# Performance work log

Hardware: AMD Instinct MI355X
Metric: run time of the kernel (lower is better)

Reference implementation:

```python
import jax, jax.numpy as jnp
import numpy as np

D_MODEL = 1024
NUM_SLOTS = 4096
MIN_K = 8
MAX_K = 32


def setup_inputs() -> dict:
    key = jax.random.key(0)
    k1, k2, k3 = jax.random.split(key, 3)
    x = jax.random.normal(k1, (4, 1024, D_MODEL), dtype=jnp.float32)
    param_pool = 0.02 * jax.random.normal(k2, (NUM_SLOTS, D_MODEL), dtype=jnp.float32)
    w_router = 0.02 * jax.random.normal(k3, (D_MODEL, NUM_SLOTS), dtype=jnp.float32)
    return {"x": x, "param_pool": param_pool, "w_router": w_router}


def _route(x, w_router):
    # Router: linear projection to slot logits, softmax, dynamic top-k in [MIN_K, MAX_K].
    logits = jnp.einsum('bsd,dn->bsn', x, w_router)           # [B,S,N]
    probs = jax.nn.softmax(logits, axis=-1)
    top_probs, indices = jax.lax.top_k(probs, MAX_K)          # [B,S,K]
    # dynamic k: always keep first MIN_K slots; keep up to MAX_K while prob > uniform
    pos = jnp.arange(MAX_K)
    keep = (pos < MIN_K) | (top_probs > (1.0 / NUM_SLOTS))    # [B,S,K] bool
    keep_f = keep.astype(top_probs.dtype)
    masked = top_probs * keep_f
    weights = masked / (jnp.sum(masked, axis=-1, keepdims=True) + 1e-9)
    # load-balancing aux loss: N * sum(mean_prob_per_slot * frac_tokens_routed_per_slot)
    mean_probs = jnp.mean(probs, axis=(0, 1))                 # [N]
    counts = jnp.zeros((NUM_SLOTS,), dtype=jnp.float32).at[indices.reshape(-1)].add(keep_f.reshape(-1))
    frac = counts / (jnp.sum(keep_f) + 1e-9)
    aux_loss = NUM_SLOTS * jnp.sum(mean_probs * frac)
    return indices, weights, keep, aux_loss


def reference(x, param_pool, w_router):
    indices, weights, keep, aux_loss = _route(x, w_router)
    selected_params = param_pool[indices]                      # [B,S,K,D] gather
    proj = jnp.einsum('bsd,bskd->bsk', x, selected_params)     # per-token dot scores
    weighted_proj = proj * weights
    output = jnp.einsum('bsk,bskd->bsd', weighted_proj, selected_params)
    flat_indices = indices.reshape(-1)
    flat_keep = keep.reshape(-1)
    touched = jnp.zeros((NUM_SLOTS,), dtype=jnp.bool_).at[flat_indices].max(flat_keep)
    active_count = jnp.sum(touched)
    return (output, aux_loss, active_count)
```

## Files before the change

kernel.cpp:

```cpp
#include <hip/hip_runtime.h>
#include <math.h>
#include <stdint.h>

#define D_MODEL   1024
#define NUM_SLOTS 4096
#define N_TOKENS  4096
#define MIN_K     8
#define MAX_K     32
#define KP        1024
#define NSTEP     32

typedef _Float16 f16x8 __attribute__((ext_vector_type(8)));
typedef _Float16 f16x4 __attribute__((ext_vector_type(4)));
typedef _Float16 h2    __attribute__((ext_vector_type(2)));
typedef float    f32x4 __attribute__((ext_vector_type(4)));

__device__ __forceinline__ void gload16(const void* g, void* l) {
    __builtin_amdgcn_global_load_lds((const __attribute__((address_space(1))) void*)g,
                                     (__attribute__((address_space(3))) void*)l,
                                     16, 0, 0);
}

__device__ __forceinline__ h2 as_h2(uint32_t u) {
    union { uint32_t u; h2 h; } c; c.u = u; return c.h;
}
__device__ __forceinline__ uint32_t h2pack(float a, float b) {
    union { uint32_t u; h2 h; } c; c.h.x = (_Float16)a; c.h.y = (_Float16)b; return c.u;
}

__device__ __forceinline__ uint32_t ford(float f) {
    uint32_t b = __float_as_uint(f);
    return b ^ (uint32_t)(((int32_t)b >> 31) | 0x80000000);
}

__global__ __launch_bounds__(256) void pack_all(const float* __restrict__ x,
                                                const float* __restrict__ w,
                                                const float* __restrict__ pool,
                                                _Float16* __restrict__ A,
                                                _Float16* __restrict__ BT,
                                                uint32_t* __restrict__ poolh,
                                                float* __restrict__ clr,
                                                int* __restrict__ failcnt) {
    __shared__ float tile[64][65];
    const int bid = blockIdx.x;
    const int tid = threadIdx.x;

    if (bid < 4096) {
        if (bid < 32) clr[bid * 256 + tid] = 0.f;
        if (bid == 32 && tid == 0) { failcnt[0] = 0; failcnt[1] = 0; }
        const int i = bid * 256 + tid;
        const float4 v = reinterpret_cast<const float4*>(x)[i];
        const int t = i >> 8;
        const int d = (i & 255) << 2;
        f16x4 hi;
        hi[0] = (_Float16)v.x; hi[1] = (_Float16)v.y;
        hi[2] = (_Float16)v.z; hi[3] = (_Float16)v.w;
        *(f16x4*)(A + (size_t)t * KP + d) = hi;
    } else if (bid < 5120) {
        const int b2 = bid - 4096;
        const int n0 = (b2 & 63) * 64;
        const int k0 = (b2 >> 6) * 64;
        {
            const int c  = tid & 63;
            const int r0 = tid >> 6;
#pragma unroll
            for (int i = 0; i < 16; ++i) {
                const int r = r0 * 16 + i;
                tile[r][c] = w[(size_t)(k0 + r) * NUM_SLOTS + n0 + c];
            }
        }
        __syncthreads();
        const int nl  = tid >> 2;
        const int kl0 = (tid & 3) * 16;
        _Float16* rowp = BT + (size_t)(n0 + nl) * KP + k0;
#pragma unroll
        for (int j4 = 0; j4 < 16; j4 += 4) {
            f16x4 hi;
#pragma unroll
            for (int u = 0; u < 4; ++u)
                hi[u] = (_Float16)tile[kl0 + j4 + u][nl];
            *(f16x4*)(rowp + kl0 + j4) = hi;
        }
    } else {
        const size_t i = (size_t)(bid - 5120) * 256 + tid;
        const float4* s4 = reinterpret_cast<const float4*>(pool);
        const float4 a = s4[2 * i];
        const float4 b = s4[2 * i + 1];
        uint4 u;
        u.x = h2pack(a.x, a.y);
        u.y = h2pack(a.z, a.w);
        u.z = h2pack(b.x, b.y);
        u.w = h2pack(b.z, b.w);
        reinterpret_cast<uint4*>(poolh)[i] = u;
    }
}

#define STAGE_A(NXT, S2) \
    gload16(gA0 + (size_t)(S2) * 32, (void*)(AsF + (NXT) * 8192 + tid * 8)); \
    gload16(gA1 + (size_t)(S2) * 32, (void*)(AsF + (NXT) * 8192 + 4096 + tid * 8));
#define STAGE_B(NXT, S2) \
    gload16(gB0 + (size_t)(S2) * 32, (void*)(BsF + (NXT) * 8192 + tid * 8)); \
    gload16(gB1 + (size_t)(S2) * 32, (void*)(BsF + (NXT) * 8192 + 4096 + tid * 8));

#define MM(AF, M) \
    acc[M][0] = __builtin_amdgcn_mfma_f32_16x16x32_f16(AF, bf0, acc[M][0], 0, 0, 0); \
    acc[M][1] = __builtin_amdgcn_mfma_f32_16x16x32_f16(AF, bf1, acc[M][1], 0, 0, 0); \
    acc[M][2] = __builtin_amdgcn_mfma_f32_16x16x32_f16(AF, bf2, acc[M][2], 0, 0, 0); \
    acc[M][3] = __builtin_amdgcn_mfma_f32_16x16x32_f16(AF, bf3, acc[M][3], 0, 0, 0);

#define GSTEP(S, CUR, NXT) do { \
    const _Float16* a_ = AsF + (CUR) * 8192; \
    const _Float16* b_ = BsF + (CUR) * 8192; \
    f16x8 bf0 = *(const f16x8*)(b_ + offB0); \
    f16x8 bf1 = *(const f16x8*)(b_ + offB1); \
    f16x8 bf2 = *(const f16x8*)(b_ + offB2); \
    f16x8 bf3 = *(const f16x8*)(b_ + offB3); \
    f16x8 a0 = *(const f16x8*)(a_ + offA0); \
    f16x8 a1 = *(const f16x8*)(a_ + offA1); \
    f16x8 a2 = *(const f16x8*)(a_ + offA2); \
    f16x8 a3 = *(const f16x8*)(a_ + offA3); \
    if ((S) + 2 < NSTEP) { STAGE_A(NXT, (S) + 2) } \
    asm volatile("" ::: "memory"); \
    __builtin_amdgcn_s_barrier(); \
    __builtin_amdgcn_s_setprio(1); \
    MM(a0, 0) MM(a1, 1) MM(a2, 2) MM(a3, 3) \
    __builtin_amdgcn_s_setprio(0); \
    asm volatile("" ::: "memory"); \
    __builtin_amdgcn_s_barrier(); \
    a0 = *(const f16x8*)(a_ + offA4); \
    a1 = *(const f16x8*)(a_ + offA5); \
    a2 = *(const f16x8*)(a_ + offA6); \
    a3 = *(const f16x8*)(a_ + offA7); \
    if ((S) + 2 < NSTEP) { STAGE_B(NXT, (S) + 2) } \
    asm volatile("" ::: "memory"); \
    __builtin_amdgcn_s_barrier(); \
    __builtin_amdgcn_s_setprio(1); \
    MM(a0, 4) MM(a1, 5) MM(a2, 6) MM(a3, 7) \
    __builtin_amdgcn_s_setprio(0); \
    if ((S) < NSTEP - 2) { asm volatile("s_waitcnt vmcnt(4)" ::: "memory"); } \
    else                 { asm volatile("s_waitcnt vmcnt(0)" ::: "memory"); } \
    __builtin_amdgcn_s_barrier(); \
} while (0)

__global__ __launch_bounds__(512, 2) void gemm256(const _Float16* __restrict__ A,
                                                  const _Float16* __restrict__ BT,
                                                  float* __restrict__ C,
                                                  int nbm) {
    __shared__ _Float16 AsF[4 * 8192];
    __shared__ _Float16 BsF[4 * 8192];
    const int tid  = threadIdx.x;
    const int lane = tid & 63;
    const int wv   = tid >> 6;
    const int wm   = wv >> 2;
    const int wn   = wv & 3;

    int brow, bcol;
    {
        const int bid = blockIdx.x;
        if (nbm == 16) {
            const int xcd = bid & 7;
            const int l   = bid >> 3;
            brow = (xcd & 3) * 4 + (l & 3);
            bcol = (xcd >> 2) * 8 + (l >> 2);
        } else {
            brow = bid >> 4;
            bcol = bid & 15;
        }
    }
    const size_t bm = (size_t)brow * 256;
    const size_t bn = (size_t)bcol * 256;

    const int rowA = tid >> 2;
    const int slot = tid & 3;
    const int sswz = slot ^ ((rowA >> 1) & 3);
    const _Float16* gA0 = A  + (bm + rowA) * (size_t)KP + sswz * 8;
    const _Float16* gA1 = A  + (bm + rowA + 128) * (size_t)KP + sswz * 8;
    const _Float16* gB0 = BT + (bn + rowA) * (size_t)KP + sswz * 8;
    const _Float16* gB1 = BT + (bn + rowA + 128) * (size_t)KP + sswz * 8;

    int offA0, offA1, offA2, offA3, offA4, offA5, offA6, offA7;
    int offB0, offB1, offB2, offB3;
    {
        const int r15 = lane & 15, ls = lane >> 4;
#define AOFF(M) (((wm) * 128 + (M) * 16 + r15) * 32 + \
                 ((ls ^ ((((wm) * 128 + (M) * 16 + r15) >> 1) & 3)) * 8))
#define BOFF(N) (((wn) * 64 + (N) * 16 + r15) * 32 + \
                 ((ls ^ ((((wn) * 64 + (N) * 16 + r15) >> 1) & 3)) * 8))
        offA0 = AOFF(0); offA1 = AOFF(1); offA2 = AOFF(2); offA3 = AOFF(3);
        offA4 = AOFF(4); offA5 = AOFF(5); offA6 = AOFF(6); offA7 = AOFF(7);
        offB0 = BOFF(0); offB1 = BOFF(1); offB2 = BOFF(2); offB3 = BOFF(3);
#undef AOFF
#undef BOFF
    }

    f32x4 acc[8][4] = {};

    STAGE_A(0, 0) STAGE_B(0, 0)
    STAGE_A(1, 1) STAGE_B(1, 1)
    asm volatile("s_waitcnt vmcnt(4)" ::: "memory");
    __builtin_amdgcn_s_barrier();

    for (int s4 = 0; s4 < NSTEP; s4 += 4) {
        GSTEP(s4 + 0, 0, 2);
        GSTEP(s4 + 1, 1, 3);
        GSTEP(s4 + 2, 2, 0);
        GSTEP(s4 + 3, 3, 1);
    }

    const size_t crow = bm + wm * 128 + ((lane >> 4) << 2);
    const size_t ccol = bn + wn * 64 + (lane & 15);
#pragma unroll
    for (int m = 0; m < 8; ++m)
#pragma unroll
        for (int r = 0; r < 4; ++r) {
            float* cp = C + (crow + m * 16 + r) * (size_t)NUM_SLOTS + ccol;
#pragma unroll
            for (int n = 0; n < 4; ++n) cp[n * 16] = acc[m][n][r];
        }
}

#define RECOMP(G, A, B, Cc, D) do { \
    uint32_t t0 = (msk & (1u << (A)))  ? k##A  : 0u; \
    uint32_t t1 = (msk & (1u << (B)))  ? k##B  : 0u; \
    uint32_t t2 = (msk & (1u << (Cc))) ? k##Cc : 0u; \
    uint32_t t3 = (msk & (1u << (D)))  ? k##D  : 0u; \
    t0 = t0 > t1 ? t0 : t1; t2 = t2 > t3 ? t2 : t3; \
    gm##G = t0 > t2 ? t0 : t2; } while (0)

#define XROUND(IT) do { \
    uint32_t best = gm0; \
    if (gm1 > best) best = gm1; \
    if (gm2 > best) best = gm2; \
    if (gm3 > best) best = gm3; \
    uint32_t wb = best; \
    _Pragma("unroll") \
    for (int o = 32; o; o >>= 1) { \
        const uint32_t p = __shfl_xor(wb, o); \
        if (p > wb) wb = p; \
    } \
    if (lane == (IT)) kept = wb; \
    if (best == wb) { \
        const int idx = 4095 - (int)(wb & 0xFFFu); \
        const int rem = idx - kb; \
        const int jj = rem >> 8; \
        msk &= ~(1u << (4 * jj + (rem & 3))); \
        switch (jj) { \
            case 0:  RECOMP(0, 0, 1, 2, 3); break; \
            case 1:  RECOMP(1, 4, 5, 6, 7); break; \
            case 2:  RECOMP(2, 8, 9, 10, 11); break; \
            default: RECOMP(3, 12, 13, 14, 15); break; \
        } \
    } \
} while (0)

#define MAKEKEYS(E0, E1, E2, E3) \
    k0  = (ford((E0).x) & 0xFFFFF000u) | (uint32_t)(4095 - (kb + 0)); \
    k1  = (ford((E0).y) & 0xFFFFF000u) | (uint32_t)(4095 - (kb + 1)); \
    k2  = (ford((E0).z) & 0xFFFFF000u) | (uint32_t)(4095 - (kb + 2)); \
    k3  = (ford((E0).w) & 0xFFFFF000u) | (uint32_t)(4095 - (kb + 3)); \
    k4  = (ford((E1).x) & 0xFFFFF000u) | (uint32_t)(4095 - (kb + 256)); \
    k5  = (ford((E1).y) & 0xFFFFF000u) | (uint32_t)(4095 - (kb + 257)); \
    k6  = (ford((E1).z) & 0xFFFFF000u) | (uint32_t)(4095 - (kb + 258)); \
    k7  = (ford((E1).w) & 0xFFFFF000u) | (uint32_t)(4095 - (kb + 259)); \
    k8  = (ford((E2).x) & 0xFFFFF000u) | (uint32_t)(4095 - (kb + 512)); \
    k9  = (ford((E2).y) & 0xFFFFF000u) | (uint32_t)(4095 - (kb + 513)); \
    k10 = (ford((E2).z) & 0xFFFFF000u) | (uint32_t)(4095 - (kb + 514)); \
    k11 = (ford((E2).w) & 0xFFFFF000u) | (uint32_t)(4095 - (kb + 515)); \
    k12 = (ford((E3).x) & 0xFFFFF000u) | (uint32_t)(4095 - (kb + 768)); \
    k13 = (ford((E3).y) & 0xFFFFF000u) | (uint32_t)(4095 - (kb + 769)); \
    k14 = (ford((E3).z) & 0xFFFFF000u) | (uint32_t)(4095 - (kb + 770)); \
    k15 = (ford((E3).w) & 0xFFFFF000u) | (uint32_t)(4095 - (kb + 771));

#define PROJ_AND_OUT(TOK) do { \
    const uint4* xA = reinterpret_cast<const uint4*>(Af + (size_t)(TOK) * D_MODEL); \
    const uint4 xq0 = xA[lane]; \
    const uint4 xq1 = xA[lane + 64]; \
    const h2 xh0 = as_h2(xq0.x), xh1 = as_h2(xq0.y); \
    const h2 xh2 = as_h2(xq0.z), xh3 = as_h2(xq0.w); \
    const h2 xh4 = as_h2(xq1.x), xh5 = as_h2(xq1.y); \
    const h2 xh6 = as_h2(xq1.z), xh7 = as_h2(xq1.w); \
    float4 oa0 = {0,0,0,0}, ob0 = {0,0,0,0}, oa1 = {0,0,0,0}, ob1 = {0,0,0,0}; \
    _Pragma("unroll") \
    for (int ii = 0; ii < 8; ++ii) { \
        const int   i     = w * 8 + ii; \
        const int   slotg = __shfl(slotv, i); \
        const float wgt   = __shfl(wgtl, i); \
        if (wgt != 0.f) { \
            const uint4* pr = reinterpret_cast<const uint4*>(poolh + (size_t)slotg * (D_MODEL / 2)); \
            const uint4 q0 = pr[lane]; \
            const uint4 q1 = pr[lane + 64]; \
            const h2 p0 = as_h2(q0.x), p1 = as_h2(q0.y); \
            const h2 p2 = as_h2(q0.z), p3 = as_h2(q0.w); \
            const h2 p4 = as_h2(q1.x), p5 = as_h2(q1.y); \
            const h2 p6 = as_h2(q1.z), p7 = as_h2(q1.w); \
            h2 acc2 = xh0 * p0; \
            acc2 = xh1 * p1 + acc2; \
            acc2 = xh2 * p2 + acc2; \
            acc2 = xh3 * p3 + acc2; \
            acc2 = xh4 * p4 + acc2; \
            acc2 = xh5 * p5 + acc2; \
            acc2 = xh6 * p6 + acc2; \
            acc2 = xh7 * p7 + acc2; \
            float d = (float)acc2.x + (float)acc2.y; \
            _Pragma("unroll") \
            for (int o = 32; o; o >>= 1) d += __shfl_xor(d, o); \
            const float wp = d * wgt; \
            oa0.x = fmaf(wp, (float)p0.x, oa0.x); oa0.y = fmaf(wp, (float)p0.y, oa0.y); \
            oa0.z = fmaf(wp, (float)p1.x, oa0.z); oa0.w = fmaf(wp, (float)p1.y, oa0.w); \
            ob0.x = fmaf(wp, (float)p2.x, ob0.x); ob0.y = fmaf(wp, (float)p2.y, ob0.y); \
            ob0.z = fmaf(wp, (float)p3.x, ob0.z); ob0.w = fmaf(wp, (float)p3.y, ob0.w); \
            oa1.x = fmaf(wp, (float)p4.x, oa1.x); oa1.y = fmaf(wp, (float)p4.y, oa1.y); \
            oa1.z = fmaf(wp, (float)p5.x, oa1.z); oa1.w = fmaf(wp, (float)p5.y, oa1.w); \
            ob1.x = fmaf(wp, (float)p6.x, ob1.x); ob1.y = fmaf(wp, (float)p6.y, ob1.y); \
            ob1.z = fmaf(wp, (float)p7.x, ob1.z); ob1.w = fmaf(wp, (float)p7.y, ob1.w); \
        } \
    } \
    { \
        float4* op = reinterpret_cast<float4*>(s_union + w * 1024); \
        op[2 * lane]       = oa0; \
        op[2 * lane + 1]   = ob0; \
        op[2 * lane + 128] = oa1; \
        op[2 * lane + 129] = ob1; \
    } \
    __syncthreads(); \
    float4 r = {0, 0, 0, 0}; \
    _Pragma("unroll") \
    for (int ww = 0; ww < 4; ++ww) { \
        const float4 vv = reinterpret_cast<const float4*>(s_union + ww * 1024)[tid]; \
        r.x += vv.x; r.y += vv.y; r.z += vv.z; r.w += vv.w; \
    } \
    reinterpret_cast<float4*>(out + (size_t)(TOK) * D_MODEL)[tid] = r; \
} while (0)

__global__ __launch_bounds__(256) void router_kernel(
    const float* __restrict__ logits,
    const _Float16* __restrict__ Af,
    const uint32_t* __restrict__ poolh,
    float* __restrict__ out,
    float2* __restrict__ minv,
    float* __restrict__ counts,
    int* __restrict__ failcnt,
    int* __restrict__ faillist) {
    __shared__ float    s_union[NUM_SLOTS];
    __shared__ uint32_t s_cand[68];
    __shared__ float    s_redv[4];

    const int tid  = threadIdx.x;
    const int w    = tid >> 6;
    const int lane = tid & 63;
    const int wseg = w << 10;
    const int t    = blockIdx.x;

    const float4* lrow4 =
        reinterpret_cast<const float4*>(logits + (size_t)t * NUM_SLOTS + wseg);

    float4 lv0, lv1, lv2, lv3;
    lv0 = lrow4[lane];
    lv1 = lrow4[lane + 64];
    lv2 = lrow4[lane + 128];
    lv3 = lrow4[lane + 192];
    reinterpret_cast<float4*>(s_union + wseg)[lane]       = lv0;
    reinterpret_cast<float4*>(s_union + wseg)[lane + 64]  = lv1;
    reinterpret_cast<float4*>(s_union + wseg)[lane + 128] = lv2;
    reinterpret_cast<float4*>(s_union + wseg)[lane + 192] = lv3;
    float lmax = fmaxf(fmaxf(fmaxf(lv0.x, lv0.y), fmaxf(lv0.z, lv0.w)),
                       fmaxf(fmaxf(lv1.x, lv1.y), fmaxf(lv1.z, lv1.w)));
    lmax = fmaxf(lmax, fmaxf(fmaxf(lv2.x, lv2.y), fmaxf(lv2.z, lv2.w)));
    lmax = fmaxf(lmax, fmaxf(fmaxf(lv3.x, lv3.y), fmaxf(lv3.z, lv3.w)));
#pragma unroll
    for (int o = 32; o; o >>= 1) lmax = fmaxf(lmax, __shfl_xor(lmax, o));
    if (lane == 0) s_redv[w] = lmax;
    __syncthreads();
    const float m = fmaxf(fmaxf(s_redv[0], s_redv[1]), fmaxf(s_redv[2], s_redv[3]));
    __syncthreads();

    float lsum;
    {
        float4 ev0, ev1, ev2, ev3;
        ev0.x = __expf(lv0.x - m); ev0.y = __expf(lv0.y - m);
        ev0.z = __expf(lv0.z - m); ev0.w = __expf(lv0.w - m);
        ev1.x = __expf(lv1.x - m); ev1.y = __expf(lv1.y - m);
        ev1.z = __expf(lv1.z - m); ev1.w = __expf(lv1.w - m);
        ev2.x = __expf(lv2.x - m); ev2.y = __expf(lv2.y - m);
        ev2.z = __expf(lv2.z - m); ev2.w = __expf(lv2.w - m);
        ev3.x = __expf(lv3.x - m); ev3.y = __expf(lv3.y - m);
        ev3.z = __expf(lv3.z - m); ev3.w = __expf(lv3.w - m);
        lsum = (ev0.x + ev0.y + ev0.z + ev0.w) + (ev1.x + ev1.y + ev1.z + ev1.w) +
               (ev2.x + ev2.y + ev2.z + ev2.w) + (ev3.x + ev3.y + ev3.z + ev3.w);
    }
#pragma unroll
    for (int o = 32; o; o >>= 1) lsum += __shfl_xor(lsum, o);
    if (lane == 0) s_redv[w] = lsum;
    __syncthreads();
    const float inv = 1.0f / (s_redv[0] + s_redv[1] + s_redv[2] + s_redv[3]);
    if (tid == 0) minv[t] = make_float2(m, inv);

    const int kb = wseg + 4 * lane;
    uint32_t k0, k1, k2, k3, k4, k5, k6, k7;
    uint32_t k8, k9, k10, k11, k12, k13, k14, k15;
    MAKEKEYS(lv0, lv1, lv2, lv3)

    uint32_t msk = 0xFFFFu;
    uint32_t gm0, gm1, gm2, gm3;
    RECOMP(0, 0, 1, 2, 3); RECOMP(1, 4, 5, 6, 7);
    RECOMP(2, 8, 9, 10, 11); RECOMP(3, 12, 13, 14, 15);

    uint32_t kept = 0;
    for (int it = 0; it < 16; ++it) { XROUND(it); }

    {
        uint32_t best = gm0;
        if (gm1 > best) best = gm1;
        if (gm2 > best) best = gm2;
        if (gm3 > best) best = gm3;
#pragma unroll
        for (int o = 32; o; o >>= 1) {
            const uint32_t p = __shfl_xor(best, o);
            if (p > best) best = p;
        }
        if (lane == 0) s_cand[64 + w] = best;
    }
    if (lane < 16) s_cand[w * 16 + lane] = kept;
    __syncthreads();

    uint32_t v0 = s_cand[lane];
#pragma unroll
    for (int k = 2; k <= 64; k <<= 1) {
#pragma unroll
        for (int j = k >> 1; j > 0; j >>= 1) {
            const bool jl = (lane & j) == 0;
            const uint32_t p = __shfl_xor(v0, j);
            const bool km = ((lane & k) == 0) == jl;
            v0 = ((p > v0) == km) ? p : v0;
        }
    }

    const uint32_t th = __shfl(v0, 31);
    uint32_t mw = s_cand[64];
    {
        const uint32_t m1 = s_cand[65], m2 = s_cand[66], m3 = s_cand[67];
        if (m1 > mw) mw = m1;
        if (m2 > mw) mw = m2;
        if (m3 > mw) mw = m3;
    }
    if (th < mw) {
        if (tid == 0) {
            const int fi = atomicAdd(failcnt, 1);
            faillist[fi] = t;
        }
        return;
    }

    const int slotv = 4095 - (int)(v0 & 0xFFFu);
    float pv = 0.f;
    if (lane < 32) pv = __expf(s_union[slotv] - m) * inv;
    const bool kp = (lane < MIN_K) || (pv > (1.0f / 4096.0f));
    float wsum = kp ? pv : 0.f;
#pragma unroll
    for (int o = 32; o; o >>= 1) wsum += __shfl_xor(wsum, o);
    const float wgtl = kp ? pv / (wsum + 1e-9f) : 0.f;
    if (w == 0 && lane < 32 && kp) atomicAdd(&counts[slotv], 1.0f);
    __syncthreads();

    PROJ_AND_OUT(t);
}

__global__ __launch_bounds__(256) void router_fixup(
    const float* __restrict__ logits,
    const _Float16* __restrict__ Af,
    const uint32_t* __restrict__ poolh,
    float* __restrict__ out,
    const float2* __restrict__ minv,
    float* __restrict__ counts,
    const int* __restrict__ failcnt,
    const int* __restrict__ faillist) {
    __shared__ float    s_union[NUM_SLOTS];
    __shared__ uint32_t s_cand[128];

    const int tid  = threadIdx.x;
    const int w    = tid >> 6;
    const int lane = tid & 63;
    const int wseg = w << 10;
    const int n    = failcnt[0];

    for (int fi = blockIdx.x; fi < n; fi += gridDim.x) {
        const int t = faillist[fi];
        const float4* lrow4 =
            reinterpret_cast<const float4*>(logits + (size_t)t * NUM_SLOTS + wseg);
        const float4 lv0 = lrow4[lane];
        const float4 lv1 = lrow4[lane + 64];
        const float4 lv2 = lrow4[lane + 128];
        const float4 lv3 = lrow4[lane + 192];
        reinterpret_cast<float4*>(s_union + wseg)[lane]       = lv0;
        reinterpret_cast<float4*>(s_union + wseg)[lane + 64]  = lv1;
        reinterpret_cast<float4*>(s_union + wseg)[lane + 128] = lv2;
        reinterpret_cast<float4*>(s_union + wseg)[lane + 192] = lv3;
        const float2 mv = minv[t];
        const float m = mv.x, inv = mv.y;

        const int kb = wseg + 4 * lane;
        uint32_t k0, k1, k2, k3, k4, k5, k6, k7;
        uint32_t k8, k9, k10, k11, k12, k13, k14, k15;
        MAKEKEYS(lv0, lv1, lv2, lv3)

        uint32_t msk = 0xFFFFu;
        uint32_t gm0, gm1, gm2, gm3;
        RECOMP(0, 0, 1, 2, 3); RECOMP(1, 4, 5, 6, 7);
        RECOMP(2, 8, 9, 10, 11); RECOMP(3, 12, 13, 14, 15);

        uint32_t kept = 0;
        for (int it = 0; it < 32; ++it) { XROUND(it); }
        if (lane < 32) s_cand[w * 32 + lane] = kept;
        __syncthreads();

        uint32_t v0 = s_cand[lane];
        uint32_t v1 = s_cand[64 + lane];
#pragma unroll
        for (int k = 2; k <= 128; k <<= 1) {
#pragma unroll
            for (int j = k >> 1; j > 0; j >>= 1) {
                if (j == 64) {
                    const uint32_t a = v0 > v1 ? v0 : v1;
                    const uint32_t b = v0 > v1 ? v1 : v0;
                    v0 = a; v1 = b;
                } else {
                    const bool jl = (lane & j) == 0;
                    {
                        const uint32_t p = __shfl_xor(v0, j);
                        const bool km = ((lane & k) == 0) == jl;
                        v0 = ((p > v0) == km) ? p : v0;
                    }
                    {
                        const uint32_t p = __shfl_xor(v1, j);
                        const bool km = (((lane + 64) & k) == 0) == jl;
                        v1 = ((p > v1) == km) ? p : v1;
                    }
                }
            }
        }

        const int slotv = 4095 - (int)(v0 & 0xFFFu);
        float pv = 0.f;
        if (lane < 32) pv = __expf(s_union[slotv] - m) * inv;
        const bool kp = (lane < MIN_K) || (pv > (1.0f / 4096.0f));
        float wsum = kp ? pv : 0.f;
#pragma unroll
        for (int o = 32; o; o >>= 1) wsum += __shfl_xor(wsum, o);
        const float wgtl = kp ? pv / (wsum + 1e-9f) : 0.f;
        if (w == 0 && lane < 32 && kp) atomicAdd(&counts[slotv], 1.0f);
        __syncthreads();

        PROJ_AND_OUT(t);
        __syncthreads();
    }
}

__global__ __launch_bounds__(256) void colsum_lg(const float* __restrict__ logits,
                                                 const float2* __restrict__ minv,
                                                 float* __restrict__ colsum) {
    const int tid = threadIdx.x;
    const int s0  = blockIdx.x * 1024;
    const int t0  = blockIdx.y * 64;
    float a0 = 0.f, a1 = 0.f, a2 = 0.f, a3 = 0.f;
    for (int t = 0; t < 64; ++t) {
        const float2 mv = minv[t0 + t];
        const float4 v = reinterpret_cast<const float4*>(
            logits + (size_t)(t0 + t) * NUM_SLOTS + s0)[tid];
        a0 = fmaf(__expf(v.x - mv.x), mv.y, a0);
        a1 = fmaf(__expf(v.y - mv.x), mv.y, a1);
        a2 = fmaf(__expf(v.z - mv.x), mv.y, a2);
        a3 = fmaf(__expf(v.w - mv.x), mv.y, a3);
    }
    const int c = s0 + 4 * tid;
    atomicAdd(&colsum[c + 0], a0);
    atomicAdd(&colsum[c + 1], a1);
    atomicAdd(&colsum[c + 2], a2);
    atomicAdd(&colsum[c + 3], a3);
}

__global__ __launch_bounds__(256) void finalize_kernel(
    const float* __restrict__ counts,
    const float* __restrict__ colsum,
    float* __restrict__ out2) {
    __shared__ float s_tot[4], s_act[4], s_dot[4];
    const int tid = threadIdx.x;
    float tot = 0.f, act = 0.f, dot = 0.f;
#pragma unroll
    for (int j = 0; j < 16; ++j) {
        const int i = j * 256 + tid;
        const float c = counts[i];
        tot += c;
        act += (c > 0.f) ? 1.f : 0.f;
        dot += colsum[i] * c;
    }
#pragma unroll
    for (int o = 32; o; o >>= 1) {
        tot += __shfl_xor(tot, o);
        act += __shfl_xor(act, o);
        dot += __shfl_xor(dot, o);
    }
    if ((tid & 63) == 0) {
        s_tot[tid >> 6] = tot; s_act[tid >> 6] = act; s_dot[tid >> 6] = dot;
    }
    __syncthreads();
    if (tid == 0) {
        const float T  = s_tot[0] + s_tot[1] + s_tot[2] + s_tot[3];
        const float A  = s_act[0] + s_act[1] + s_act[2] + s_act[3];
        const float Dt = s_dot[0] + s_dot[1] + s_dot[2] + s_dot[3];
        out2[0] = Dt / (T + 1e-9f);
        out2[1] = A;
    }
}

extern "C" void kernel_launch(void* const* d_in, const int* in_sizes, int n_in,
                              void* d_out, int out_size, void* d_ws, size_t ws_size,
                              hipStream_t stream) {
    const float* x    = (const float*)d_in[0];
    const float* pool = (const float*)d_in[1];
    const float* w    = (const float*)d_in[2];
    float* out = (float*)d_out;

    const size_t MB = 1024 * 1024;
    char* ws = (char*)d_ws;
    float*     colsum   = (float*)ws;
    float*     counts   = (float*)(ws + 16 * 1024);
    float2*    minv     = (float2*)(ws + 32 * 1024);
    int*       failcnt  = (int*)(ws + 64 * 1024);
    int*       faillist = (int*)(ws + 68 * 1024);
    uint32_t*  poolh    = (uint32_t*)(ws + 128 * 1024);
    _Float16*  Apack    = (_Float16*)(ws + 128 * 1024 + 8 * MB);
    _Float16*  Bpack    = (_Float16*)(ws + 128 * 1024 + 16 * MB);
    float*     logits   = (float*)(ws + 128 * 1024 + 24 * MB);

    pack_all<<<7168, 256, 0, stream>>>(x, w, pool, Apack, Bpack, poolh,
                                       colsum, failcnt);

    gemm256<<<16 * 16, 512, 0, stream>>>(Apack, Bpack, logits, 16);

    router_kernel<<<N_TOKENS, 256, 0, stream>>>(logits, Apack, poolh, out,
                                                minv, counts, failcnt, faillist);

    router_fixup<<<64, 256, 0, stream>>>(logits, Apack, poolh, out,
                                         minv, counts, failcnt, faillist);

    colsum_lg<<<dim3(NUM_SLOTS / 1024, N_TOKENS / 64), 256, 0, stream>>>(
        logits, minv, colsum);

    finalize_kernel<<<1, 256, 0, stream>>>(counts, colsum, out + (out_size - 2));
}
```

Measured before the change: 149.7 us.

## Store router logits as fp16 and merge fixup with finalize kernel

The GEMM now writes the 4096x4096 logits matrix in fp16 instead of fp32, which halves the write traffic and the later reads by the router and colsum kernels. The fixup kernel is merged with the finalize step using a last-block atomic counter, removing one launch. colsum now runs before fixup. Storing logits in fp16 costs precision, which can change top-k selection among near-tied probabilities and alter the softmax values.

Measured after the change: 146.2 us. 2.4% less time.

```diff
diff --git a/kernel.cpp b/kernel.cpp
--- a/kernel.cpp
+++ b/kernel.cpp
@@ -144,7 +144,7 @@
 
 __global__ __launch_bounds__(512, 2) void gemm256(const _Float16* __restrict__ A,
                                                   const _Float16* __restrict__ BT,
-                                                  float* __restrict__ C,
+                                                  _Float16* __restrict__ C,
                                                   int nbm) {
     __shared__ _Float16 AsF[4 * 8192];
     __shared__ _Float16 BsF[4 * 8192];
@@ -213,9 +213,9 @@
     for (int m = 0; m < 8; ++m)
 #pragma unroll
         for (int r = 0; r < 4; ++r) {
-            float* cp = C + (crow + m * 16 + r) * (size_t)NUM_SLOTS + ccol;
-#pragma unroll
-            for (int n = 0; n < 4; ++n) cp[n * 16] = acc[m][n][r];
+            _Float16* cp = C + (crow + m * 16 + r) * (size_t)NUM_SLOTS + ccol;
+#pragma unroll
+            for (int n = 0; n < 4; ++n) cp[n * 16] = (_Float16)acc[m][n][r];
         }
 }
 
@@ -252,6 +252,25 @@
         } \
     } \
 } while (0)
+
+#define LOADLV(TOK) \
+    const uint2* lrow2 = reinterpret_cast<const uint2*>(logits + (size_t)(TOK) * NUM_SLOTS + wseg); \
+    float4 lv0, lv1, lv2, lv3; \
+    { \
+        const uint2 u0 = lrow2[lane]; \
+        const uint2 u1 = lrow2[lane + 64]; \
+        const uint2 u2 = lrow2[lane + 128]; \
+        const uint2 u3 = lrow2[lane + 192]; \
+        h2 ha, hb; \
+        ha = as_h2(u0.x); hb = as_h2(u0.y); \
+        lv0 = make_float4((float)ha.x, (float)ha.y, (float)hb.x, (float)hb.y); \
+        ha = as_h2(u1.x); hb = as_h2(u1.y); \
+        lv1 = make_float4((float)ha.x, (float)ha.y, (float)hb.x, (float)hb.y); \
+        ha = as_h2(u2.x); hb = as_h2(u2.y); \
+        lv2 = make_float4((float)ha.x, (float)ha.y, (float)hb.x, (float)hb.y); \
+        ha = as_h2(u3.x); hb = as_h2(u3.y); \
+        lv3 = make_float4((float)ha.x, (float)ha.y, (float)hb.x, (float)hb.y); \
+    }
 
 #define MAKEKEYS(E0, E1, E2, E3) \
     k0  = (ford((E0).x) & 0xFFFFF000u) | (uint32_t)(4095 - (kb + 0)); \
@@ -333,7 +352,7 @@
 } while (0)
 
 __global__ __launch_bounds__(256) void router_kernel(
-    const float* __restrict__ logits,
+    const _Float16* __restrict__ logits,
     const _Float16* __restrict__ Af,
     const uint32_t* __restrict__ poolh,
     float* __restrict__ out,
@@ -351,14 +370,8 @@
     const int wseg = w << 10;
     const int t    = blockIdx.x;
 
-    const float4* lrow4 =
-        reinterpret_cast<const float4*>(logits + (size_t)t * NUM_SLOTS + wseg);
-
-    float4 lv0, lv1, lv2, lv3;
-    lv0 = lrow4[lane];
-    lv1 = lrow4[lane + 64];
-    lv2 = lrow4[lane + 128];
-    lv3 = lrow4[lane + 192];
+    LOADLV(t)
+
     reinterpret_cast<float4*>(s_union + wseg)[lane]       = lv0;
     reinterpret_cast<float4*>(s_union + wseg)[lane + 64]  = lv1;
     reinterpret_cast<float4*>(s_union + wseg)[lane + 128] = lv2;
@@ -465,17 +478,45 @@
     PROJ_AND_OUT(t);
 }
 
-__global__ __launch_bounds__(256) void router_fixup(
-    const float* __restrict__ logits,
+__global__ __launch_bounds__(256) void colsum_lg(const _Float16* __restrict__ logits,
+                                                 const float2* __restrict__ minv,
+                                                 float* __restrict__ colsum) {
+    const int tid = threadIdx.x;
+    const int s0  = blockIdx.x * 1024;
+    const int t0  = blockIdx.y * 64;
+    float a0 = 0.f, a1 = 0.f, a2 = 0.f, a3 = 0.f;
+    for (int t = 0; t < 64; ++t) {
+        const float2 mv = minv[t0 + t];
+        const uint2 v = reinterpret_cast<const uint2*>(
+            logits + (size_t)(t0 + t) * NUM_SLOTS + s0)[tid];
+        const h2 va = as_h2(v.x), vb = as_h2(v.y);
+        a0 = fmaf(__expf((float)va.x - mv.x), mv.y, a0);
+        a1 = fmaf(__expf((float)va.y - mv.x), mv.y, a1);
+        a2 = fmaf(__expf((float)vb.x - mv.x), mv.y, a2);
+        a3 = fmaf(__expf((float)vb.y - mv.x), mv.y, a3);
+    }
+    const int c = s0 + 4 * tid;
+    atomicAdd(&colsum[c + 0], a0);
+    atomicAdd(&colsum[c + 1], a1);
+    atomicAdd(&colsum[c + 2], a2);
+    atomicAdd(&colsum[c + 3], a3);
+}
+
+__global__ __launch_bounds__(256) void fixup_fin(
+    const _Float16* __restrict__ logits,
     const _Float16* __restrict__ Af,
     const uint32_t* __restrict__ poolh,
     float* __restrict__ out,
     const float2* __restrict__ minv,
     float* __restrict__ counts,
-    const int* __restrict__ failcnt,
-    const int* __restrict__ faillist) {
+    float* __restrict__ colsum,
+    int* __restrict__ failcnt,
+    const int* __restrict__ faillist,
+    float* __restrict__ out2) {
     __shared__ float    s_union[NUM_SLOTS];
     __shared__ uint32_t s_cand[128];
+    __shared__ float    s_tot[4], s_act[4], s_dot[4];
+    __shared__ int      s_last;
 
     const int tid  = threadIdx.x;
     const int w    = tid >> 6;
@@ -485,12 +526,7 @@
 
     for (int fi = blockIdx.x; fi < n; fi += gridDim.x) {
         const int t = faillist[fi];
-        const float4* lrow4 =
-            reinterpret_cast<const float4*>(logits + (size_t)t * NUM_SLOTS + wseg);
-        const float4 lv0 = lrow4[lane];
-        const float4 lv1 = lrow4[lane + 64];
-        const float4 lv2 = lrow4[lane + 128];
-        const float4 lv3 = lrow4[lane + 192];
+        LOADLV(t)
         reinterpret_cast<float4*>(s_union + wseg)[lane]       = lv0;
         reinterpret_cast<float4*>(s_union + wseg)[lane + 64]  = lv1;
         reinterpret_cast<float4*>(s_union + wseg)[lane + 128] = lv2;
@@ -553,62 +589,40 @@
         PROJ_AND_OUT(t);
         __syncthreads();
     }
-}
-
-__global__ __launch_bounds__(256) void colsum_lg(const float* __restrict__ logits,
-                                                 const float2* __restrict__ minv,
-                                                 float* __restrict__ colsum) {
-    const int tid = threadIdx.x;
-    const int s0  = blockIdx.x * 1024;
-    const int t0  = blockIdx.y * 64;
-    float a0 = 0.f, a1 = 0.f, a2 = 0.f, a3 = 0.f;
-    for (int t = 0; t < 64; ++t) {
-        const float2 mv = minv[t0 + t];
-        const float4 v = reinterpret_cast<const float4*>(
-            logits + (size_t)(t0 + t) * NUM_SLOTS + s0)[tid];
-        a0 = fmaf(__expf(v.x - mv.x), mv.y, a0);
-        a1 = fmaf(__expf(v.y - mv.x), mv.y, a1);
-        a2 = fmaf(__expf(v.z - mv.x), mv.y, a2);
-        a3 = fmaf(__expf(v.w - mv.x), mv.y, a3);
-    }
-    const int c = s0 + 4 * tid;
-    atomicAdd(&colsum[c + 0], a0);
-    atomicAdd(&colsum[c + 1], a1);
-    atomicAdd(&colsum[c + 2], a2);
-    atomicAdd(&colsum[c + 3], a3);
-}
-
-__global__ __launch_bounds__(256) void finalize_kernel(
-    const float* __restrict__ counts,
-    const float* __restrict__ colsum,
-    float* __restrict__ out2) {
-    __shared__ float s_tot[4], s_act[4], s_dot[4];
-    const int tid = threadIdx.x;
-    float tot = 0.f, act = 0.f, dot = 0.f;
-#pragma unroll
-    for (int j = 0; j < 16; ++j) {
-        const int i = j * 256 + tid;
-        const float c = counts[i];
-        tot += c;
-        act += (c > 0.f) ? 1.f : 0.f;
-        dot += colsum[i] * c;
-    }
-#pragma unroll
-    for (int o = 32; o; o >>= 1) {
-        tot += __shfl_xor(tot, o);
-        act += __shfl_xor(act, o);
-        dot += __shfl_xor(dot, o);
-    }
-    if ((tid & 63) == 0) {
-        s_tot[tid >> 6] = tot; s_act[tid >> 6] = act; s_dot[tid >> 6] = dot;
-    }
+
+    __threadfence();
     __syncthreads();
-    if (tid == 0) {
-        const float T  = s_tot[0] + s_tot[1] + s_tot[2] + s_tot[3];
-        const float A  = s_act[0] + s_act[1] + s_act[2] + s_act[3];
-        const float Dt = s_dot[0] + s_dot[1] + s_dot[2] + s_dot[3];
-        out2[0] = Dt / (T + 1e-9f);
-        out2[1] = A;
+    if (tid == 0) s_last = (atomicAdd(&failcnt[1], 1) == (int)gridDim.x - 1) ? 1 : 0;
+    __syncthreads();
+    if (s_last) {
+        __threadfence();
+        float tot = 0.f, act = 0.f, dot = 0.f;
+#pragma unroll
+        for (int j = 0; j < 16; ++j) {
+            const int i = j * 256 + tid;
+            const float c  = atomicAdd(&counts[i], 0.f);
+            const float cs = colsum[i];
+            tot += c;
+            act += (c > 0.f) ? 1.f : 0.f;
+            dot += cs * c;
+        }
+#pragma unroll
+        for (int o = 32; o; o >>= 1) {
+            tot += __shfl_xor(tot, o);
+            act += __shfl_xor(act, o);
+            dot += __shfl_xor(dot, o);
+        }
+        if ((tid & 63) == 0) {
+            s_tot[tid >> 6] = tot; s_act[tid >> 6] = act; s_dot[tid >> 6] = dot;
+        }
+        __syncthreads();
+        if (tid == 0) {
+            const float T  = s_tot[0] + s_tot[1] + s_tot[2] + s_tot[3];
+            const float A  = s_act[0] + s_act[1] + s_act[2] + s_act[3];
+            const float Dt = s_dot[0] + s_dot[1] + s_dot[2] + s_dot[3];
+            out2[0] = Dt / (T + 1e-9f);
+            out2[1] = A;
+        }
     }
 }
 
@@ -630,7 +644,7 @@
     uint32_t*  poolh    = (uint32_t*)(ws + 128 * 1024);
     _Float16*  Apack    = (_Float16*)(ws + 128 * 1024 + 8 * MB);
     _Float16*  Bpack    = (_Float16*)(ws + 128 * 1024 + 16 * MB);
-    float*     logits   = (float*)(ws + 128 * 1024 + 24 * MB);
+    _Float16*  logits   = (_Float16*)(ws + 128 * 1024 + 24 * MB);
 
     pack_all<<<7168, 256, 0, stream>>>(x, w, pool, Apack, Bpack, poolh,
                                        colsum, failcnt);
@@ -640,11 +654,10 @@
     router_kernel<<<N_TOKENS, 256, 0, stream>>>(logits, Apack, poolh, out,
                                                 minv, counts, failcnt, faillist);
 
-    router_fixup<<<64, 256, 0, stream>>>(logits, Apack, poolh, out,
-                                         minv, counts, failcnt, faillist);
-
     colsum_lg<<<dim3(NUM_SLOTS / 1024, N_TOKENS / 64), 256, 0, stream>>>(
         logits, minv, colsum);
 
-    finalize_kernel<<<1, 256, 0, stream>>>(counts, colsum, out + (out_size - 2));
-}
+    fixup_fin<<<64, 256, 0, stream>>>(logits, Apack, poolh, out, minv,
+                                      counts, colsum, failcnt, faillist,
+                                      out + (out_size - 2));
+}
```
